# Optimization experiments

Measured on AMD Instinct MI355X. Metric: run time of the kernel, lower is better.

The kernel has to match this reference:

```python
import jax, jax.numpy as jnp
import numpy as np

DIM = 1024
HEADS = 16
DIM_HEAD = DIM // HEADS  # 64


def setup_inputs() -> dict:
    key = jax.random.key(0)
    k1, k2, k3 = jax.random.split(key, 3)
    x = jax.random.normal(k1, (4, 2048, DIM), dtype=jnp.float32)
    # Linear weights stored as [in, out] so y = x @ W (torch Linear uses x @ W.T; init is random either way)
    w_qkv = jax.random.normal(k2, (DIM, 3 * DIM), dtype=jnp.float32) * (DIM ** -0.5)
    w_out = jax.random.normal(k3, (DIM, DIM), dtype=jnp.float32) * (DIM ** -0.5)
    return {"x": x, "w_qkv": w_qkv, "w_out": w_out}


def reference(x, w_qkv, w_out):
    b, t, d = x.shape
    h, dh = HEADS, DIM_HEAD
    qkv = x @ w_qkv  # [b, t, 3*h*dh]
    q, k, v = jnp.split(qkv, 3, axis=-1)
    split_heads = lambda a: a.reshape(b, t, h, dh).transpose(0, 2, 1, 3)  # [b,h,t,dh]
    q, k, v = map(split_heads, (q, k, v))
    # NOTE: original scales by full model dim d, not per-head dim
    scale = d ** (-0.5)
    dots = jnp.einsum('bhie,bhje->bhij', q, k) * scale  # [b,h,t,t]
    attn = jax.nn.softmax(dots, axis=-1)
    out = jnp.einsum('bhij,bhje->bhie', attn, v)  # [b,h,t,dh]
    out = out.transpose(0, 2, 1, 3).reshape(b, t, h * dh)
    return out @ w_out
```

## Files before the change

### kernel.cpp

```cpp
#include <hip/hip_runtime.h>


typedef __bf16 bf16x8 __attribute__((ext_vector_type(8)));
typedef __bf16 bf16x4 __attribute__((ext_vector_type(4)));
typedef __bf16 bf16x2 __attribute__((ext_vector_type(2)));
typedef float f32x4 __attribute__((ext_vector_type(4)));
typedef float f32x2 __attribute__((ext_vector_type(2)));
typedef float f32x16 __attribute__((ext_vector_type(16)));
typedef unsigned short ushort8 __attribute__((ext_vector_type(8)));

#define MFMA16(a, b, c) __builtin_amdgcn_mfma_f32_16x16x32_bf16((a), (b), (c), 0, 0, 0)
#define MFMA32(a, b, c) __builtin_amdgcn_mfma_f32_32x32x16_bf16((a), (b), (c), 0, 0, 0)

__device__ __forceinline__ unsigned short f2bf(float f) {
  unsigned int u = __float_as_uint(f);
  u = (u + 0x7FFFu + ((u >> 16) & 1u)) >> 16;
  return (unsigned short)u;
}

__device__ __forceinline__ float fast_exp2(float x) {
#if __has_builtin(__builtin_amdgcn_exp2f)
  return __builtin_amdgcn_exp2f(x);
#else
  float r;
  asm("v_exp_f32 %0, %1" : "=v"(r) : "v"(x));
  return r;
#endif
}

__device__ __forceinline__ void gload_lds16(const unsigned short* g, unsigned short* l) {
  __builtin_amdgcn_global_load_lds(
      (const __attribute__((address_space(1))) unsigned int*)g,
      (__attribute__((address_space(3))) unsigned int*)l, 16, 0, 0);
}

__device__ __forceinline__ void half_swap(unsigned int a, unsigned int b,
                                          unsigned int& x, unsigned int& y,
                                          bool H) {
#if __has_builtin(__builtin_amdgcn_permlane32_swap)
  auto r = __builtin_amdgcn_permlane32_swap(a, b, false, false);
  x = (unsigned int)r[0];
  y = (unsigned int)r[1];
#else
  unsigned int oa = (unsigned int)__shfl_xor((int)a, 32);
  unsigned int ob = (unsigned int)__shfl_xor((int)b, 32);
  x = H ? ob : a;
  y = H ? b : oa;
#endif
}

__global__ __launch_bounds__(256) void prep_kernel(
    const float* __restrict__ x, unsigned short* __restrict__ xb,
    const float* __restrict__ wqkv, unsigned short* __restrict__ WqkvT,
    const float* __restrict__ wout, unsigned short* __restrict__ WoutT) {
  const int bid = blockIdx.x;
  const int tid = threadIdx.x;
  if (bid < 4096) {
    int i = (bid * 256 + tid) * 8;
    float4 a = *(const float4*)&x[i];
    float4 b = *(const float4*)&x[i + 4];
    ushort8 o = {f2bf(a.x), f2bf(a.y), f2bf(a.z), f2bf(a.w),
                 f2bf(b.x), f2bf(b.y), f2bf(b.z), f2bf(b.w)};
    *(ushort8*)&xb[i] = o;
    return;
  }
  __shared__ float t[32][33];
  const float* in;
  unsigned short* out;
  int C, scale_limit, c0, r0;
  if (bid < 4096 + 3072) {
    int tj = bid - 4096;
    in = wqkv; out = WqkvT; C = 3072; scale_limit = 1024;
    c0 = (tj % 96) * 32; r0 = (tj / 96) * 32;
  } else {
    int tj = bid - 7168;
    in = wout; out = WoutT; C = 1024; scale_limit = 0;
    c0 = (tj & 31) * 32; r0 = (tj >> 5) * 32;
  }
  const float kQScale = 0.045084220027780106f;
#pragma unroll
  for (int i = 0; i < 4; ++i) {
    int e = tid + i * 256;
    int r = e >> 5, c = e & 31;
    t[r][c] = in[(size_t)(r0 + r) * C + c0 + c];
  }
  __syncthreads();
#pragma unroll
  for (int i = 0; i < 4; ++i) {
    int e = tid + i * 256;
    int r = e >> 5, c = e & 31;
    float v = t[c][r];
    if (c0 + r < scale_limit) v *= kQScale;
    out[(size_t)(c0 + r) * 1024 + r0 + c] = f2bf(v);
  }
}

template <int MODE>
__global__ __launch_bounds__(256) void gemm_bt(
    const unsigned short* __restrict__ A, const unsigned short* __restrict__ Bt,
    void* __restrict__ Cv, unsigned short* __restrict__ VT,
    int M, int N, int K) {
  __shared__ unsigned short As[128 * 32];
  __shared__ unsigned short Bs[128 * 32];
  const int tid = threadIdx.x;
  const int wave = tid >> 6, lane = tid & 63;
  const int g = lane >> 4, ln = lane & 15;
  const int wm = wave >> 1, wn = wave & 1;
  const long bm = (long)blockIdx.y * 128;
  const long bn = (long)blockIdx.x * 128;

  f32x4 acc[4][4];
#pragma unroll
  for (int i = 0; i < 4; ++i)
#pragma unroll
    for (int j = 0; j < 4; ++j) acc[i][j] = (f32x4){0.f, 0.f, 0.f, 0.f};

  const int srow = wave * 32 + (lane >> 2);
  const int scol = (lane & 3) * 8;
  const unsigned short* gA0 = A + (bm + srow) * (long)K + scol;
  const unsigned short* gA1 = gA0 + 16 * (long)K;
  const unsigned short* gB0 = Bt + (bn + srow) * (long)K + scol;
  const unsigned short* gB1 = gB0 + 16 * (long)K;
  unsigned short* lA0 = &As[wave * 1024];
  unsigned short* lA1 = &As[wave * 1024 + 512];
  unsigned short* lB0 = &Bs[wave * 1024];
  unsigned short* lB1 = &Bs[wave * 1024 + 512];

  for (int k0 = 0; k0 < K; k0 += 32) {
    __syncthreads();
    gload_lds16(gA0 + k0, lA0);
    gload_lds16(gA1 + k0, lA1);
    gload_lds16(gB0 + k0, lB0);
    gload_lds16(gB1 + k0, lB1);
    __syncthreads();

    bf16x8 af[4], bfr[4];
#pragma unroll
    for (int i = 0; i < 4; ++i) {
      af[i]  = *(const bf16x8*)&As[(wm * 64 + i * 16 + ln) * 32 + g * 8];
      bfr[i] = *(const bf16x8*)&Bs[(wn * 64 + i * 16 + ln) * 32 + g * 8];
    }
    __builtin_amdgcn_s_setprio(1);
#pragma unroll
    for (int i = 0; i < 4; ++i)
#pragma unroll
      for (int j = 0; j < 4; ++j)
        acc[i][j] = MFMA16(af[i], bfr[j], acc[i][j]);
    __builtin_amdgcn_s_setprio(0);
  }

  const long crow = bm + wm * 64, ccol = bn + wn * 64;
  if (MODE == 2 && bn >= 2048) {
#pragma unroll
    for (int i = 0; i < 4; ++i)
#pragma unroll
      for (int j = 0; j < 4; ++j) {
        int nv = (int)(ccol + j * 16 + ln) - 2048;
        int h = nv >> 6, dh = nv & 63;
        long tg = crow + i * 16 + g * 4;
        int b = (int)(tg >> 11), tl = (int)(tg & 2047);
        size_t idx = (size_t)(b * 16 + h) * 131072 + (size_t)dh * 2048 + tl;
        bf16x4 o = {(__bf16)acc[i][j][0], (__bf16)acc[i][j][1],
                    (__bf16)acc[i][j][2], (__bf16)acc[i][j][3]};
        *(bf16x4*)&VT[idx] = o;
      }
  } else {
#pragma unroll
    for (int i = 0; i < 4; ++i)
#pragma unroll
      for (int j = 0; j < 4; ++j)
#pragma unroll
        for (int r = 0; r < 4; ++r) {
          long idx = (crow + i * 16 + g * 4 + r) * (long)N + ccol + j * 16 + ln;
          if (MODE == 1)
            ((float*)Cv)[idx] = acc[i][j][r];
          else
            ((unsigned short*)Cv)[idx] = f2bf(acc[i][j][r]);
        }
  }
}

__global__ __launch_bounds__(256, 4) void attn_kernel(
    const unsigned short* __restrict__ qkv, const unsigned short* __restrict__ VT,
    unsigned short* __restrict__ attn_out) {
  __shared__ unsigned short Ks[2][64][64];
  __shared__ unsigned short Vs[2][64][64];

  const int tid = threadIdx.x;
  const int wave = tid >> 6, lane = tid & 63;
  const int l31 = lane & 31, hb = lane >> 5;

  const int wg = (blockIdx.x & 7) * 128 + (blockIdx.x >> 3);
  const int bh = wg >> 4, qc = wg & 15;
  const int b = bh >> 4, head = bh & 15;
  const int q0 = qc * 128 + wave * 32;

  bf16x8 qf[4];
  {
    size_t base = (size_t)(b * 2048 + q0 + l31) * 3072 + head * 64 + 8 * hb;
    qf[0] = *(const bf16x8*)&qkv[base];
    qf[1] = *(const bf16x8*)&qkv[base + 16];
    qf[2] = *(const bf16x8*)&qkv[base + 32];
    qf[3] = *(const bf16x8*)&qkv[base + 48];
  }

  f32x16 oacc[2];
#pragma unroll
  for (int i = 0; i < 16; ++i) { oacc[0][i] = 0.f; oacc[1][i] = 0.f; }
  f32x2 ls = {0.f, 0.f};

  const int srow = tid >> 3;
  const int sc = tid & 7;
  const int swz = (sc ^ (srow & 7)) * 8;
  const unsigned short* gK =
      qkv + (size_t)b * 2048 * 3072 + 1024 + head * 64 + (size_t)srow * 3072 + swz;
  const unsigned short* gV = VT + (size_t)bh * 131072 + (size_t)srow * 2048 + swz;
  const int wrow = wave * 8;

  auto STAGE = [&](int buf, int j) {
    gload_lds16(gK + (size_t)j * 3072,        &Ks[buf][wrow][0]);
    gload_lds16(gK + (size_t)(j + 32) * 3072, &Ks[buf][wrow + 32][0]);
    gload_lds16(gV + j,                       &Vs[buf][wrow][0]);
    gload_lds16(gV + 32 * 2048 + j,           &Vs[buf][wrow + 32][0]);
  };

  const int myx = l31 & 7;
  const bool H = (hb != 0);

  STAGE(0, 0);
  asm volatile("s_waitcnt vmcnt(0)" ::: "memory");
  __syncthreads();

  int cur = 0;
  for (int j0 = 0; j0 < 2048; j0 += 64) {
    if (j0 + 64 < 2048) STAGE(cur ^ 1, j0 + 64);

#pragma unroll
    for (int kt = 0; kt < 2; ++kt) {
      f32x16 sa;
#pragma unroll
      for (int i = 0; i < 16; ++i) sa[i] = 0.f;
      __builtin_amdgcn_s_setprio(1);
#pragma unroll
      for (int t = 0; t < 4; ++t) {
        bf16x8 kf = *(const bf16x8*)&Ks[cur][kt * 32 + l31][((2 * t + hb) ^ myx) * 8];
        sa = MFMA32(kf, qf[t], sa);
      }
      __builtin_amdgcn_s_setprio(0);

      unsigned int pkw[8];
#pragma unroll
      for (int j = 0; j < 8; ++j) {
        float p0 = fast_exp2(sa[2 * j]);
        float p1 = fast_exp2(sa[2 * j + 1]);
        ls += (f32x2){p0, p1};
        bf16x2 pv = {(__bf16)p0, (__bf16)p1};
        pkw[j] = __builtin_bit_cast(unsigned int, pv);
      }

      union { unsigned int u[4]; bf16x8 v; } pf0, pf1;
      half_swap(pkw[0], pkw[2], pf0.u[0], pf0.u[2], H);
      half_swap(pkw[1], pkw[3], pf0.u[1], pf0.u[3], H);
      half_swap(pkw[4], pkw[6], pf1.u[0], pf1.u[2], H);
      half_swap(pkw[5], pkw[7], pf1.u[1], pf1.u[3], H);

      __builtin_amdgcn_s_setprio(1);
#pragma unroll
      for (int mt = 0; mt < 2; ++mt) {
        bf16x8 vf0 = *(const bf16x8*)&Vs[cur][mt * 32 + l31][((4 * kt + hb) ^ myx) * 8];
        bf16x8 vf1 = *(const bf16x8*)&Vs[cur][mt * 32 + l31][((4 * kt + 2 + hb) ^ myx) * 8];
        oacc[mt] = MFMA32(vf0, pf0.v, oacc[mt]);
        oacc[mt] = MFMA32(vf1, pf1.v, oacc[mt]);
      }
      __builtin_amdgcn_s_setprio(0);
    }

    asm volatile("s_waitcnt vmcnt(0)" ::: "memory");
    __syncthreads();
    cur ^= 1;
  }

  float l = ls.x + ls.y;
  l += __shfl_xor(l, 32);
  float inv = 1.0f / l;
  size_t row = (size_t)(b * 2048 + q0 + l31) * 1024 + head * 64;
#pragma unroll
  for (int mt = 0; mt < 2; ++mt)
#pragma unroll
    for (int rq = 0; rq < 4; ++rq) {
      bf16x4 o = {(__bf16)(oacc[mt][4 * rq + 0] * inv),
                  (__bf16)(oacc[mt][4 * rq + 1] * inv),
                  (__bf16)(oacc[mt][4 * rq + 2] * inv),
                  (__bf16)(oacc[mt][4 * rq + 3] * inv)};
      *(bf16x4*)&attn_out[row + mt * 32 + 8 * rq + 4 * hb] = o;
    }
}

extern "C" void kernel_launch(void* const* d_in, const int* in_sizes, int n_in,
                              void* d_out, int out_size, void* d_ws, size_t ws_size,
                              hipStream_t stream) {
  (void)in_sizes; (void)n_in; (void)out_size; (void)ws_size;
  const float* x_f     = (const float*)d_in[0];
  const float* w_qkv_f = (const float*)d_in[1];
  const float* w_out_f = (const float*)d_in[2];
  float* out = (float*)d_out;

  char* ws = (char*)d_ws;
  unsigned short* qkv   = (unsigned short*)(ws);
  unsigned short* attn  = (unsigned short*)(ws + 50331648);
  unsigned short* VT    = (unsigned short*)(ws + 67108864);
  unsigned short* WqkvT = (unsigned short*)(ws + 83886080);
  unsigned short* WoutT = (unsigned short*)(ws + 90177536);
  unsigned short* xb    = (unsigned short*)(ws + 92274688);

  prep_kernel<<<8192, 256, 0, stream>>>(x_f, xb, w_qkv_f, WqkvT, w_out_f, WoutT);
  gemm_bt<2><<<dim3(24, 64), 256, 0, stream>>>(xb, WqkvT, qkv, VT, 8192, 3072, 1024);
  attn_kernel<<<1024, 256, 0, stream>>>(qkv, VT, attn);
  gemm_bt<1><<<dim3(8, 64), 256, 0, stream>>>(attn, WoutT, out, nullptr, 8192, 1024, 1024);
}
```

Measured before the change: 187.0 us.

## Process two 32-row query tiles per wave to reuse K/V LDS fragments

Each wave now handles 64 query rows (two 32-row tiles) instead of 32, so every K and V fragment read from LDS feeds two MFMAs. The grid halves to 512 workgroups, the block-to-tile mapping changes to cover 256 queries per block, and launch bounds drop to 2 blocks per CU to make room for the doubled accumulators. This cuts global K/V staging traffic and LDS reads per unit of work. In exchange it raises register pressure, lowers occupancy, and leaves fewer workgroups than before to spread across the CUs.

After: 184.2 us. About the same (-1.4%).

```diff
diff --git a/kernel.cpp b/kernel.cpp
--- a/kernel.cpp
+++ b/kernel.cpp
@@ -180,7 +180,7 @@
   }
 }
 
-__global__ __launch_bounds__(256, 4) void attn_kernel(
+__global__ __launch_bounds__(256, 2) void attn_kernel(
     const unsigned short* __restrict__ qkv, const unsigned short* __restrict__ VT,
     unsigned short* __restrict__ attn_out) {
   __shared__ unsigned short Ks[2][64][64];
@@ -190,24 +190,32 @@
   const int wave = tid >> 6, lane = tid & 63;
   const int l31 = lane & 31, hb = lane >> 5;
 
-  const int wg = (blockIdx.x & 7) * 128 + (blockIdx.x >> 3);
-  const int bh = wg >> 4, qc = wg & 15;
+  const int wg = (blockIdx.x & 7) * 64 + (blockIdx.x >> 3);
+  const int bh = wg >> 3, qc = wg & 7;
   const int b = bh >> 4, head = bh & 15;
-  const int q0 = qc * 128 + wave * 32;
-
-  bf16x8 qf[4];
+  const int q0 = qc * 256 + wave * 64;
+
+  bf16x8 qfA[4], qfB[4];
   {
-    size_t base = (size_t)(b * 2048 + q0 + l31) * 3072 + head * 64 + 8 * hb;
-    qf[0] = *(const bf16x8*)&qkv[base];
-    qf[1] = *(const bf16x8*)&qkv[base + 16];
-    qf[2] = *(const bf16x8*)&qkv[base + 32];
-    qf[3] = *(const bf16x8*)&qkv[base + 48];
-  }
-
-  f32x16 oacc[2];
-#pragma unroll
-  for (int i = 0; i < 16; ++i) { oacc[0][i] = 0.f; oacc[1][i] = 0.f; }
-  f32x2 ls = {0.f, 0.f};
+    size_t baseA = (size_t)(b * 2048 + q0 + l31) * 3072 + head * 64 + 8 * hb;
+    size_t baseB = baseA + (size_t)32 * 3072;
+    qfA[0] = *(const bf16x8*)&qkv[baseA];
+    qfA[1] = *(const bf16x8*)&qkv[baseA + 16];
+    qfA[2] = *(const bf16x8*)&qkv[baseA + 32];
+    qfA[3] = *(const bf16x8*)&qkv[baseA + 48];
+    qfB[0] = *(const bf16x8*)&qkv[baseB];
+    qfB[1] = *(const bf16x8*)&qkv[baseB + 16];
+    qfB[2] = *(const bf16x8*)&qkv[baseB + 32];
+    qfB[3] = *(const bf16x8*)&qkv[baseB + 48];
+  }
+
+  f32x16 oaccA[2], oaccB[2];
+#pragma unroll
+  for (int i = 0; i < 16; ++i) {
+    oaccA[0][i] = 0.f; oaccA[1][i] = 0.f;
+    oaccB[0][i] = 0.f; oaccB[1][i] = 0.f;
+  }
+  f32x2 lsA = {0.f, 0.f}, lsB = {0.f, 0.f};
 
   const int srow = tid >> 3;
   const int sc = tid & 7;
@@ -237,40 +245,52 @@
 
 #pragma unroll
     for (int kt = 0; kt < 2; ++kt) {
-      f32x16 sa;
-#pragma unroll
-      for (int i = 0; i < 16; ++i) sa[i] = 0.f;
+      f32x16 saA, saB;
+#pragma unroll
+      for (int i = 0; i < 16; ++i) { saA[i] = 0.f; saB[i] = 0.f; }
       __builtin_amdgcn_s_setprio(1);
 #pragma unroll
       for (int t = 0; t < 4; ++t) {
         bf16x8 kf = *(const bf16x8*)&Ks[cur][kt * 32 + l31][((2 * t + hb) ^ myx) * 8];
-        sa = MFMA32(kf, qf[t], sa);
+        saA = MFMA32(kf, qfA[t], saA);
+        saB = MFMA32(kf, qfB[t], saB);
       }
       __builtin_amdgcn_s_setprio(0);
 
-      unsigned int pkw[8];
+      unsigned int pkwA[8], pkwB[8];
 #pragma unroll
       for (int j = 0; j < 8; ++j) {
-        float p0 = fast_exp2(sa[2 * j]);
-        float p1 = fast_exp2(sa[2 * j + 1]);
-        ls += (f32x2){p0, p1};
-        bf16x2 pv = {(__bf16)p0, (__bf16)p1};
-        pkw[j] = __builtin_bit_cast(unsigned int, pv);
-      }
-
-      union { unsigned int u[4]; bf16x8 v; } pf0, pf1;
-      half_swap(pkw[0], pkw[2], pf0.u[0], pf0.u[2], H);
-      half_swap(pkw[1], pkw[3], pf0.u[1], pf0.u[3], H);
-      half_swap(pkw[4], pkw[6], pf1.u[0], pf1.u[2], H);
-      half_swap(pkw[5], pkw[7], pf1.u[1], pf1.u[3], H);
+        float a0 = fast_exp2(saA[2 * j]);
+        float a1 = fast_exp2(saA[2 * j + 1]);
+        lsA += (f32x2){a0, a1};
+        bf16x2 av = {(__bf16)a0, (__bf16)a1};
+        pkwA[j] = __builtin_bit_cast(unsigned int, av);
+        float b0 = fast_exp2(saB[2 * j]);
+        float b1 = fast_exp2(saB[2 * j + 1]);
+        lsB += (f32x2){b0, b1};
+        bf16x2 bv = {(__bf16)b0, (__bf16)b1};
+        pkwB[j] = __builtin_bit_cast(unsigned int, bv);
+      }
+
+      union { unsigned int u[4]; bf16x8 v; } pfA0, pfA1, pfB0, pfB1;
+      half_swap(pkwA[0], pkwA[2], pfA0.u[0], pfA0.u[2], H);
+      half_swap(pkwA[1], pkwA[3], pfA0.u[1], pfA0.u[3], H);
+      half_swap(pkwA[4], pkwA[6], pfA1.u[0], pfA1.u[2], H);
+      half_swap(pkwA[5], pkwA[7], pfA1.u[1], pfA1.u[3], H);
+      half_swap(pkwB[0], pkwB[2], pfB0.u[0], pfB0.u[2], H);
+      half_swap(pkwB[1], pkwB[3], pfB0.u[1], pfB0.u[3], H);
+      half_swap(pkwB[4], pkwB[6], pfB1.u[0], pfB1.u[2], H);
+      half_swap(pkwB[5], pkwB[7], pfB1.u[1], pfB1.u[3], H);
 
       __builtin_amdgcn_s_setprio(1);
 #pragma unroll
       for (int mt = 0; mt < 2; ++mt) {
         bf16x8 vf0 = *(const bf16x8*)&Vs[cur][mt * 32 + l31][((4 * kt + hb) ^ myx) * 8];
         bf16x8 vf1 = *(const bf16x8*)&Vs[cur][mt * 32 + l31][((4 * kt + 2 + hb) ^ myx) * 8];
-        oacc[mt] = MFMA32(vf0, pf0.v, oacc[mt]);
-        oacc[mt] = MFMA32(vf1, pf1.v, oacc[mt]);
+        oaccA[mt] = MFMA32(vf0, pfA0.v, oaccA[mt]);
+        oaccA[mt] = MFMA32(vf1, pfA1.v, oaccA[mt]);
+        oaccB[mt] = MFMA32(vf0, pfB0.v, oaccB[mt]);
+        oaccB[mt] = MFMA32(vf1, pfB1.v, oaccB[mt]);
       }
       __builtin_amdgcn_s_setprio(0);
     }
@@ -280,20 +300,38 @@
     cur ^= 1;
   }
 
-  float l = ls.x + ls.y;
-  l += __shfl_xor(l, 32);
-  float inv = 1.0f / l;
-  size_t row = (size_t)(b * 2048 + q0 + l31) * 1024 + head * 64;
-#pragma unroll
-  for (int mt = 0; mt < 2; ++mt)
-#pragma unroll
-    for (int rq = 0; rq < 4; ++rq) {
-      bf16x4 o = {(__bf16)(oacc[mt][4 * rq + 0] * inv),
-                  (__bf16)(oacc[mt][4 * rq + 1] * inv),
-                  (__bf16)(oacc[mt][4 * rq + 2] * inv),
-                  (__bf16)(oacc[mt][4 * rq + 3] * inv)};
-      *(bf16x4*)&attn_out[row + mt * 32 + 8 * rq + 4 * hb] = o;
-    }
+  {
+    float l = lsA.x + lsA.y;
+    l += __shfl_xor(l, 32);
+    float inv = 1.0f / l;
+    size_t row = (size_t)(b * 2048 + q0 + l31) * 1024 + head * 64;
+#pragma unroll
+    for (int mt = 0; mt < 2; ++mt)
+#pragma unroll
+      for (int rq = 0; rq < 4; ++rq) {
+        bf16x4 o = {(__bf16)(oaccA[mt][4 * rq + 0] * inv),
+                    (__bf16)(oaccA[mt][4 * rq + 1] * inv),
+                    (__bf16)(oaccA[mt][4 * rq + 2] * inv),
+                    (__bf16)(oaccA[mt][4 * rq + 3] * inv)};
+        *(bf16x4*)&attn_out[row + mt * 32 + 8 * rq + 4 * hb] = o;
+      }
+  }
+  {
+    float l = lsB.x + lsB.y;
+    l += __shfl_xor(l, 32);
+    float inv = 1.0f / l;
+    size_t row = (size_t)(b * 2048 + q0 + 32 + l31) * 1024 + head * 64;
+#pragma unroll
+    for (int mt = 0; mt < 2; ++mt)
+#pragma unroll
+      for (int rq = 0; rq < 4; ++rq) {
+        bf16x4 o = {(__bf16)(oaccB[mt][4 * rq + 0] * inv),
+                    (__bf16)(oaccB[mt][4 * rq + 1] * inv),
+                    (__bf16)(oaccB[mt][4 * rq + 2] * inv),
+                    (__bf16)(oaccB[mt][4 * rq + 3] * inv)};
+        *(bf16x4*)&attn_out[row + mt * 32 + 8 * rq + 4 * hb] = o;
+      }
+  }
 }
 
 extern "C" void kernel_launch(void* const* d_in, const int* in_sizes, int n_in,
@@ -315,6 +353,6 @@
 
   prep_kernel<<<8192, 256, 0, stream>>>(x_f, xb, w_qkv_f, WqkvT, w_out_f, WoutT);
   gemm_bt<2><<<dim3(24, 64), 256, 0, stream>>>(xb, WqkvT, qkv, VT, 8192, 3072, 1024);
-  attn_kernel<<<1024, 256, 0, stream>>>(qkv, VT, attn);
+  attn_kernel<<<512, 256, 0, stream>>>(qkv, VT, attn);
   gemm_bt<1><<<dim3(8, 64), 256, 0, stream>>>(attn, WoutT, out, nullptr, 8192, 1024, 1024);
 }
```

## Shrink attention blocks to two waves and drop LDS double buffering

Applied to the files above, without the earlier changes.

The attention kernel now runs 2048 blocks of 128 threads, each covering 64 query rows, where before it ran 1024 blocks of 256 threads. The K/V LDS tiles are single-buffered, so each iteration loads the tile, waits, and syncs before computing. Each block uses half the LDS, which is meant to fit more independent blocks per CU and let them hide each other's load latency. The cost is that no block overlaps its own loads with compute any more, and each K/V tile is fetched by twice as many blocks.

New measurement: 192.7 us. +3.1%, slower.

```diff
diff --git a/kernel.cpp b/kernel.cpp
--- a/kernel.cpp
+++ b/kernel.cpp
@@ -180,20 +180,20 @@
   }
 }
 
-__global__ __launch_bounds__(256, 4) void attn_kernel(
+__global__ __launch_bounds__(128, 4) void attn_kernel(
     const unsigned short* __restrict__ qkv, const unsigned short* __restrict__ VT,
     unsigned short* __restrict__ attn_out) {
-  __shared__ unsigned short Ks[2][64][64];
-  __shared__ unsigned short Vs[2][64][64];
+  __shared__ unsigned short Ks[64][64];
+  __shared__ unsigned short Vs[64][64];
 
   const int tid = threadIdx.x;
   const int wave = tid >> 6, lane = tid & 63;
   const int l31 = lane & 31, hb = lane >> 5;
 
-  const int wg = (blockIdx.x & 7) * 128 + (blockIdx.x >> 3);
-  const int bh = wg >> 4, qc = wg & 15;
+  const int wg = (blockIdx.x & 7) * 256 + (blockIdx.x >> 3);
+  const int bh = wg >> 5, qc = wg & 31;
   const int b = bh >> 4, head = bh & 15;
-  const int q0 = qc * 128 + wave * 32;
+  const int q0 = qc * 64 + wave * 32;
 
   bf16x8 qf[4];
   {
@@ -209,31 +209,32 @@
   for (int i = 0; i < 16; ++i) { oacc[0][i] = 0.f; oacc[1][i] = 0.f; }
   f32x2 ls = {0.f, 0.f};
 
-  const int srow = tid >> 3;
-  const int sc = tid & 7;
-  const int swz = (sc ^ (srow & 7)) * 8;
-  const unsigned short* gK =
-      qkv + (size_t)b * 2048 * 3072 + 1024 + head * 64 + (size_t)srow * 3072 + swz;
-  const unsigned short* gV = VT + (size_t)bh * 131072 + (size_t)srow * 2048 + swz;
-  const int wrow = wave * 8;
-
-  auto STAGE = [&](int buf, int j) {
-    gload_lds16(gK + (size_t)j * 3072,        &Ks[buf][wrow][0]);
-    gload_lds16(gK + (size_t)(j + 32) * 3072, &Ks[buf][wrow + 32][0]);
-    gload_lds16(gV + j,                       &Vs[buf][wrow][0]);
-    gload_lds16(gV + 32 * 2048 + j,           &Vs[buf][wrow + 32][0]);
-  };
+  const int srow0 = wave * 8 + (lane >> 3);
+  const int sch = lane & 7;
+  unsigned short* ldsK = &((unsigned short*)Ks)[wave * 512];
+  unsigned short* ldsV = &((unsigned short*)Vs)[wave * 512];
+  const unsigned short* gKL[4];
+  const unsigned short* gVL[4];
+#pragma unroll
+  for (int L = 0; L < 4; ++L) {
+    int row = srow0 + 16 * L;
+    int swc = (sch ^ (row & 7)) * 8;
+    gKL[L] = qkv + (size_t)b * 6291456 + 1024 + head * 64 + (size_t)row * 3072 + swc;
+    gVL[L] = VT + (size_t)bh * 131072 + (size_t)row * 2048 + swc;
+  }
 
   const int myx = l31 & 7;
   const bool H = (hb != 0);
 
-  STAGE(0, 0);
-  asm volatile("s_waitcnt vmcnt(0)" ::: "memory");
-  __syncthreads();
-
-  int cur = 0;
   for (int j0 = 0; j0 < 2048; j0 += 64) {
-    if (j0 + 64 < 2048) STAGE(cur ^ 1, j0 + 64);
+    __syncthreads();
+#pragma unroll
+    for (int L = 0; L < 4; ++L) {
+      gload_lds16(gKL[L] + (size_t)j0 * 3072, ldsK + L * 1024);
+      gload_lds16(gVL[L] + j0,                ldsV + L * 1024);
+    }
+    asm volatile("s_waitcnt vmcnt(0)" ::: "memory");
+    __syncthreads();
 
 #pragma unroll
     for (int kt = 0; kt < 2; ++kt) {
@@ -243,7 +244,7 @@
       __builtin_amdgcn_s_setprio(1);
 #pragma unroll
       for (int t = 0; t < 4; ++t) {
-        bf16x8 kf = *(const bf16x8*)&Ks[cur][kt * 32 + l31][((2 * t + hb) ^ myx) * 8];
+        bf16x8 kf = *(const bf16x8*)&Ks[kt * 32 + l31][((2 * t + hb) ^ myx) * 8];
         sa = MFMA32(kf, qf[t], sa);
       }
       __builtin_amdgcn_s_setprio(0);
@@ -267,17 +268,13 @@
       __builtin_amdgcn_s_setprio(1);
 #pragma unroll
       for (int mt = 0; mt < 2; ++mt) {
-        bf16x8 vf0 = *(const bf16x8*)&Vs[cur][mt * 32 + l31][((4 * kt + hb) ^ myx) * 8];
-        bf16x8 vf1 = *(const bf16x8*)&Vs[cur][mt * 32 + l31][((4 * kt + 2 + hb) ^ myx) * 8];
+        bf16x8 vf0 = *(const bf16x8*)&Vs[mt * 32 + l31][((4 * kt + hb) ^ myx) * 8];
+        bf16x8 vf1 = *(const bf16x8*)&Vs[mt * 32 + l31][((4 * kt + 2 + hb) ^ myx) * 8];
         oacc[mt] = MFMA32(vf0, pf0.v, oacc[mt]);
         oacc[mt] = MFMA32(vf1, pf1.v, oacc[mt]);
       }
       __builtin_amdgcn_s_setprio(0);
     }
-
-    asm volatile("s_waitcnt vmcnt(0)" ::: "memory");
-    __syncthreads();
-    cur ^= 1;
   }
 
   float l = ls.x + ls.y;
@@ -315,6 +312,6 @@
 
   prep_kernel<<<8192, 256, 0, stream>>>(x_f, xb, w_qkv_f, WqkvT, w_out_f, WoutT);
   gemm_bt<2><<<dim3(24, 64), 256, 0, stream>>>(xb, WqkvT, qkv, VT, 8192, 3072, 1024);
-  attn_kernel<<<1024, 256, 0, stream>>>(qkv, VT, attn);
+  attn_kernel<<<2048, 128, 0, stream>>>(qkv, VT, attn);
   gemm_bt<1><<<dim3(8, 64), 256, 0, stream>>>(attn, WoutT, out, nullptr, 8192, 1024, 1024);
 }
```
